# Performance work log

Measured on AMD Instinct MI355X. Metric: run time of the kernel, lower is better.

The kernel has to match this reference:

```python
import jax, jax.numpy as jnp
import numpy as np

NEIGHBOR_K = 3

def setup_inputs() -> dict:
    key = jax.random.key(0)
    k1, k2 = jax.random.split(key)
    query_fea = jax.random.normal(k1, (8, 75, 121, 640), dtype=jnp.float32)
    support_fea = jax.random.normal(k2, (8, 5, 5, 121, 640), dtype=jnp.float32)
    return {"query_fea": query_fea, "support_fea": support_fea}

def reference(query_fea, support_fea):
    # query_fea: [b, n_wq, patch_num, dim]
    # support_fea: [b, way, shot, patch_num, dim]
    b, way, shot, pn, dim = support_fea.shape
    sup = support_fea.reshape(b, way, shot * pn, dim)  # [b, way, S, dim]
    # inner products between every query patch and every support patch
    # sim: [b, n_wq, way, patch_num, S]
    sim = jnp.einsum('bqpd,bwsd->bqwps', query_fea, sup)
    # top-k over support patches (last axis), then mean over all topk values
    topk = jax.lax.top_k(sim, NEIGHBOR_K)[0]  # [b, n_wq, way, patch_num, k]
    return jnp.mean(topk, axis=(-2, -1))  # [b, n_wq, way]
```

## Files before the change

kernel.cpp:

```cpp
#include <hip/hip_runtime.h>
#include <hip/hip_bf16.h>

#define BATCH 8
#define NQ    75
#define WAY   5
#define PN    121
#define DIM   640
#define SSZ   605
#define TOPK  3

#define TM 128
#define TN 128
#define BK 64
#define NCH 5
#define KCH 10
#define QSTR 72

#define WSQ_ELEMS ((size_t)BATCH * NQ * TM * DIM)
#define WSS_ELEMS ((size_t)BATCH * WAY * 640 * DIM)
#define WS_NEED   ((WSQ_ELEMS + WSS_ELEMS) * 2)

typedef __attribute__((ext_vector_type(8))) short   short8;
typedef __attribute__((ext_vector_type(8))) __bf16  bf16x8;
typedef __attribute__((ext_vector_type(4))) float   f32x4;

__device__ inline unsigned short f2bf(float f) {
  unsigned u = __builtin_bit_cast(unsigned, f);
  return (unsigned short)((u + 0x7fffu + ((u >> 16) & 1u)) >> 16);
}

__device__ inline void ins3(float &a, float &b, float &c, float v) {
  float na = fmaxf(a, v);
  float nb = __builtin_amdgcn_fmed3f(v, a, b);
  float nc2 = __builtin_amdgcn_fmed3f(v, b, c);
  a = na; b = nb; c = nc2;
}


__global__ __launch_bounds__(256) void cvt_q(const float* __restrict__ qf,
                                             unsigned short* __restrict__ dst) {
  int idx = blockIdx.x * 256 + threadIdx.x;
  int c4  = idx % 160;
  int row = (idx / 160) & 127;
  int bq  = idx / (160 * 128);
  float4 v = make_float4(0.f, 0.f, 0.f, 0.f);
  if (row < PN)
    v = *reinterpret_cast<const float4*>(qf + ((size_t)(bq * PN + row) * DIM + c4 * 4));
  ushort4 h;
  h.x = f2bf(v.x); h.y = f2bf(v.y); h.z = f2bf(v.z); h.w = f2bf(v.w);
  *reinterpret_cast<ushort4*>(dst + (size_t)idx * 4) = h;
}

__global__ __launch_bounds__(256) void cvt_s(const float* __restrict__ sf,
                                             unsigned short* __restrict__ dst) {
  int idx = blockIdx.x * 256 + threadIdx.x;
  int c4  = idx % 160;
  int row = (idx / 160) % 640;
  int bw  = idx / (160 * 640);
  float4 v = make_float4(0.f, 0.f, 0.f, 0.f);
  if (row < SSZ)
    v = *reinterpret_cast<const float4*>(sf + ((size_t)(bw * SSZ + row) * DIM + c4 * 4));
  ushort4 h;
  h.x = f2bf(v.x); h.y = f2bf(v.y); h.z = f2bf(v.z); h.w = f2bf(v.w);
  *reinterpret_cast<ushort4*>(dst + (size_t)idx * 4) = h;
}


__global__ __launch_bounds__(256) void lpc_main(
    const short* __restrict__ wq,
    const short* __restrict__ wsp,
    float* __restrict__ out)
{
  __shared__ short Qs[TM][QSTR];
  __shared__ short Ss[TN][QSTR];
  __shared__ float t3row[TM][TOPK];
  __shared__ float red[4];

  const int bid = blockIdx.x;
  const int w   = bid % WAY;
  const int bq  = bid / WAY;
  const int b   = bid / (WAY * NQ);

  const short* Qb = wq  + (size_t)bq * TM * DIM;
  const short* Sb = wsp + (size_t)(b * WAY + w) * 640 * DIM;

  const int tid  = threadIdx.x;
  const int lane = tid & 63;
  const int wv   = tid >> 6;
  const int l15  = lane & 15;
  const int quad = lane >> 4;

  float t0[2][4], t1[2][4], t2[2][4];
  #pragma unroll
  for (int mt = 0; mt < 2; ++mt)
    #pragma unroll
    for (int r = 0; r < 4; ++r) {
      t0[mt][r] = -3.0e38f; t1[mt][r] = -3.0e38f; t2[mt][r] = -3.0e38f;
    }

  for (int nc = 0; nc < NCH; ++nc) {
    f32x4 acc[2][8];
    #pragma unroll
    for (int mt = 0; mt < 2; ++mt)
      #pragma unroll
      for (int nt = 0; nt < 8; ++nt)
        acc[mt][nt] = (f32x4){0.f, 0.f, 0.f, 0.f};

    for (int kc = 0; kc < KCH; ++kc) {
      const int kbase = kc * BK;
      __syncthreads();

      #pragma unroll
      for (int i = 0; i < 4; ++i) {
        int lin = i * 256 + tid;
        int row = lin >> 3;
        int ch  = lin & 7;
        float4 v = *reinterpret_cast<const float4*>(Qb + (size_t)row * DIM + kbase + ch * 8);
        *reinterpret_cast<float4*>(&Qs[row][ch * 8]) = v;
      }
      #pragma unroll
      for (int i = 0; i < 4; ++i) {
        int lin = i * 256 + tid;
        int row = lin >> 3;
        int ch  = lin & 7;
        float4 v = *reinterpret_cast<const float4*>(Sb + (size_t)(nc * TN + row) * DIM + kbase + ch * 8);
        *reinterpret_cast<float4*>(&Ss[row][ch * 8]) = v;
      }
      __syncthreads();

      #pragma unroll
      for (int kk = 0; kk < 2; ++kk) {
        bf16x8 a0 = __builtin_bit_cast(bf16x8,
            *reinterpret_cast<const short8*>(&Qs[wv * 32 +  0 + l15][kk * 32 + quad * 8]));
        bf16x8 a1 = __builtin_bit_cast(bf16x8,
            *reinterpret_cast<const short8*>(&Qs[wv * 32 + 16 + l15][kk * 32 + quad * 8]));
        #pragma unroll
        for (int nt = 0; nt < 8; ++nt) {
          bf16x8 bb = __builtin_bit_cast(bf16x8,
              *reinterpret_cast<const short8*>(&Ss[nt * 16 + l15][kk * 32 + quad * 8]));
          acc[0][nt] = __builtin_amdgcn_mfma_f32_16x16x32_bf16(a0, bb, acc[0][nt], 0, 0, 0);
          acc[1][nt] = __builtin_amdgcn_mfma_f32_16x16x32_bf16(a1, bb, acc[1][nt], 0, 0, 0);
        }
      }
    }

    #pragma unroll
    for (int nt = 0; nt < 8; ++nt) {
      int col = nc * TN + nt * 16 + l15;
      bool valid = col < SSZ;
      #pragma unroll
      for (int mt = 0; mt < 2; ++mt)
        #pragma unroll
        for (int r = 0; r < 4; ++r) {
          float v = valid ? acc[mt][nt][r] : -3.0e38f;
          ins3(t0[mt][r], t1[mt][r], t2[mt][r], v);
        }
    }
  }

  #pragma unroll
  for (int m = 1; m < 16; m <<= 1) {
    #pragma unroll
    for (int mt = 0; mt < 2; ++mt)
      #pragma unroll
      for (int r = 0; r < 4; ++r) {
        float o0 = __shfl_xor(t0[mt][r], m);
        float o1 = __shfl_xor(t1[mt][r], m);
        float o2 = __shfl_xor(t2[mt][r], m);
        ins3(t0[mt][r], t1[mt][r], t2[mt][r], o0);
        ins3(t0[mt][r], t1[mt][r], t2[mt][r], o1);
        ins3(t0[mt][r], t1[mt][r], t2[mt][r], o2);
      }
  }
  __syncthreads();
  if (l15 == 0) {
    #pragma unroll
    for (int mt = 0; mt < 2; ++mt)
      #pragma unroll
      for (int r = 0; r < 4; ++r) {
        int row = wv * 32 + mt * 16 + quad * 4 + r;
        t3row[row][0] = t0[mt][r];
        t3row[row][1] = t1[mt][r];
        t3row[row][2] = t2[mt][r];
      }
  }
  __syncthreads();

  float s = 0.f;
  for (int i = tid; i < PN * TOPK; i += 256)
    s += t3row[i / TOPK][i % TOPK];
  #pragma unroll
  for (int off = 32; off > 0; off >>= 1)
    s += __shfl_down(s, off);
  if (lane == 0) red[wv] = s;
  __syncthreads();
  if (tid == 0)
    out[bid] = (red[0] + red[1] + red[2] + red[3]) * (1.0f / (PN * TOPK));
}


#define FTN 64
#define FQSTR 72
#define FCSTR 67

__global__ __launch_bounds__(256) void lpc_fallback(
    const float* __restrict__ qf, const float* __restrict__ sf,
    float* __restrict__ out)
{
  __shared__ short Qs[TM][FQSTR];
  __shared__ short Ss[FTN][FQSTR];
  __shared__ float Cs[TM][FCSTR];
  __shared__ float top3[TM][TOPK];
  __shared__ float red[4];

  const int bid = blockIdx.x;
  const int w   = bid % WAY;
  const int qi  = (bid / WAY) % NQ;
  const int b   = bid / (WAY * NQ);
  const float* Qb = qf + ((size_t)(b * NQ + qi)) * PN * DIM;
  const float* Sb = sf + ((size_t)(b * WAY + w)) * SSZ * DIM;
  const int tid  = threadIdx.x;
  const int lane = tid & 63;
  const int wv   = tid >> 6;
  const int l15  = lane & 15;
  const int quad = lane >> 4;

  if (tid < TM) { top3[tid][0] = -3.0e38f; top3[tid][1] = -3.0e38f; top3[tid][2] = -3.0e38f; }
  f32x4 acc[2][4];
  for (int nc = 0; nc < 10; ++nc) {
    const int sbase = nc * FTN;
    int vn = SSZ - sbase; if (vn > FTN) vn = FTN;
    #pragma unroll
    for (int mt = 0; mt < 2; ++mt)
      #pragma unroll
      for (int nt = 0; nt < 4; ++nt) acc[mt][nt] = (f32x4){0.f,0.f,0.f,0.f};
    for (int kc = 0; kc < KCH; ++kc) {
      const int kbase = kc * BK;
      __syncthreads();
      #pragma unroll
      for (int i = 0; i < 8; ++i) {
        int lin = i * 256 + tid; int row = lin >> 4; int c4 = lin & 15;
        float4 v = make_float4(0.f,0.f,0.f,0.f);
        if (row < PN) v = *reinterpret_cast<const float4*>(Qb + (size_t)row * DIM + kbase + c4 * 4);
        ushort4 h; h.x=f2bf(v.x); h.y=f2bf(v.y); h.z=f2bf(v.z); h.w=f2bf(v.w);
        *reinterpret_cast<ushort4*>(&Qs[row][c4*4]) = h;
      }
      #pragma unroll
      for (int i = 0; i < 4; ++i) {
        int lin = i * 256 + tid; int row = lin >> 4; int c4 = lin & 15;
        int srow = sbase + row;
        float4 v = make_float4(0.f,0.f,0.f,0.f);
        if (srow < SSZ) v = *reinterpret_cast<const float4*>(Sb + (size_t)srow * DIM + kbase + c4 * 4);
        ushort4 h; h.x=f2bf(v.x); h.y=f2bf(v.y); h.z=f2bf(v.z); h.w=f2bf(v.w);
        *reinterpret_cast<ushort4*>(&Ss[row][c4*4]) = h;
      }
      __syncthreads();
      #pragma unroll
      for (int kk = 0; kk < 2; ++kk) {
        bf16x8 a0 = __builtin_bit_cast(bf16x8, *reinterpret_cast<const short8*>(&Qs[wv*32+ 0+l15][kk*32+quad*8]));
        bf16x8 a1 = __builtin_bit_cast(bf16x8, *reinterpret_cast<const short8*>(&Qs[wv*32+16+l15][kk*32+quad*8]));
        #pragma unroll
        for (int nt = 0; nt < 4; ++nt) {
          bf16x8 bb = __builtin_bit_cast(bf16x8, *reinterpret_cast<const short8*>(&Ss[nt*16+l15][kk*32+quad*8]));
          acc[0][nt] = __builtin_amdgcn_mfma_f32_16x16x32_bf16(a0, bb, acc[0][nt], 0,0,0);
          acc[1][nt] = __builtin_amdgcn_mfma_f32_16x16x32_bf16(a1, bb, acc[1][nt], 0,0,0);
        }
      }
    }
    #pragma unroll
    for (int mt = 0; mt < 2; ++mt)
      #pragma unroll
      for (int nt = 0; nt < 4; ++nt)
        #pragma unroll
        for (int r = 0; r < 4; ++r)
          Cs[wv*32+mt*16+quad*4+r][nt*16+l15] = acc[mt][nt][r];
    __syncthreads();
    {
      int row = tid >> 1; int half = tid & 1;
      float a = -3.0e38f, bb2 = -3.0e38f, c = -3.0e38f;
      int c0 = half * 32; int cend = c0 + 32; if (cend > vn) cend = vn;
      for (int cc = c0; cc < cend; ++cc) ins3(a, bb2, c, Cs[row][cc]);
      float o0 = __shfl_xor(a,1), o1 = __shfl_xor(bb2,1), o2 = __shfl_xor(c,1);
      ins3(a,bb2,c,o0); ins3(a,bb2,c,o1); ins3(a,bb2,c,o2);
      if (half == 0) {
        float r0=top3[row][0], r1=top3[row][1], r2=top3[row][2];
        ins3(r0,r1,r2,a); ins3(r0,r1,r2,bb2); ins3(r0,r1,r2,c);
        top3[row][0]=r0; top3[row][1]=r1; top3[row][2]=r2;
      }
    }
    __syncthreads();
  }
  float s = 0.f;
  for (int i = tid; i < PN * TOPK; i += 256) s += top3[i/TOPK][i%TOPK];
  #pragma unroll
  for (int off = 32; off > 0; off >>= 1) s += __shfl_down(s, off);
  if (lane == 0) red[wv] = s;
  __syncthreads();
  if (tid == 0) out[bid] = (red[0]+red[1]+red[2]+red[3]) * (1.0f/(PN*TOPK));
}


extern "C" void kernel_launch(void* const* d_in, const int* in_sizes, int n_in,
                              void* d_out, int out_size, void* d_ws, size_t ws_size,
                              hipStream_t stream) {
  const float* qf = (const float*)d_in[0];
  const float* sf = (const float*)d_in[1];
  float* out = (float*)d_out;
  (void)in_sizes; (void)n_in; (void)out_size;

  if (ws_size >= WS_NEED && d_ws != nullptr) {
    unsigned short* wq = (unsigned short*)d_ws;
    unsigned short* ws = wq + WSQ_ELEMS;
    cvt_q<<<48000, 256, 0, stream>>>(qf, wq);
    cvt_s<<<16000, 256, 0, stream>>>(sf, ws);
    lpc_main<<<BATCH * NQ * WAY, 256, 0, stream>>>((const short*)wq, (const short*)ws, out);
  } else {
    lpc_fallback<<<BATCH * NQ * WAY, 256, 0, stream>>>(qf, sf, out);
  }
}
```

Baseline: 773.4 us.

## Pre-swizzle bf16 tiles and stream them to LDS via direct global-to-LDS loads

```diff
diff --git a/kernel.cpp b/kernel.cpp
--- a/kernel.cpp
+++ b/kernel.cpp
@@ -9,16 +9,14 @@
 #define SSZ   605
 #define TOPK  3
 
-#define TM 128
-#define TN 128
-#define BK 64
+#define KCH 10
 #define NCH 5
-#define KCH 10
-#define QSTR 72
-
-#define WSQ_ELEMS ((size_t)BATCH * NQ * TM * DIM)
-#define WSS_ELEMS ((size_t)BATCH * WAY * 640 * DIM)
-#define WS_NEED   ((WSQ_ELEMS + WSS_ELEMS) * 2)
+
+#define NQCH  (600 * 10 * 128 * 8)
+#define NSCH  (40 * 5 * 10 * 128 * 8)
+#define TOTCH (NQCH + NSCH)
+#define WSQ_BYTES ((size_t)NQCH * 16)
+#define WS_NEED   ((size_t)TOTCH * 16)
 
 typedef __attribute__((ext_vector_type(8))) short   short8;
 typedef __attribute__((ext_vector_type(8))) __bf16  bf16x8;
@@ -30,50 +28,69 @@
 }
 
 __device__ inline void ins3(float &a, float &b, float &c, float v) {
-  float na = fmaxf(a, v);
-  float nb = __builtin_amdgcn_fmed3f(v, a, b);
+  float na  = fmaxf(a, v);
+  float nb  = __builtin_amdgcn_fmed3f(v, a, b);
   float nc2 = __builtin_amdgcn_fmed3f(v, b, c);
   a = na; b = nb; c = nc2;
 }
 
-
-__global__ __launch_bounds__(256) void cvt_q(const float* __restrict__ qf,
-                                             unsigned short* __restrict__ dst) {
+__device__ inline void async_copy16(const void* g, void* l) {
+  __builtin_amdgcn_global_load_lds(
+      (const __attribute__((address_space(1))) unsigned int*)g,
+      (__attribute__((address_space(3))) unsigned int*)l, 16, 0, 0);
+}
+
+__global__ __launch_bounds__(256) void cvt_pack(const float* __restrict__ qf,
+                                                const float* __restrict__ sf,
+                                                unsigned short* __restrict__ wq,
+                                                unsigned short* __restrict__ wsp) {
   int idx = blockIdx.x * 256 + threadIdx.x;
-  int c4  = idx % 160;
-  int row = (idx / 160) & 127;
-  int bq  = idx / (160 * 128);
-  float4 v = make_float4(0.f, 0.f, 0.f, 0.f);
-  if (row < PN)
-    v = *reinterpret_cast<const float4*>(qf + ((size_t)(bq * PN + row) * DIM + c4 * 4));
-  ushort4 h;
-  h.x = f2bf(v.x); h.y = f2bf(v.y); h.z = f2bf(v.z); h.w = f2bf(v.w);
-  *reinterpret_cast<ushort4*>(dst + (size_t)idx * 4) = h;
-}
-
-__global__ __launch_bounds__(256) void cvt_s(const float* __restrict__ sf,
-                                             unsigned short* __restrict__ dst) {
-  int idx = blockIdx.x * 256 + threadIdx.x;
-  int c4  = idx % 160;
-  int row = (idx / 160) % 640;
-  int bw  = idx / (160 * 640);
-  float4 v = make_float4(0.f, 0.f, 0.f, 0.f);
-  if (row < SSZ)
-    v = *reinterpret_cast<const float4*>(sf + ((size_t)(bw * SSZ + row) * DIM + c4 * 4));
-  ushort4 h;
-  h.x = f2bf(v.x); h.y = f2bf(v.y); h.z = f2bf(v.z); h.w = f2bf(v.w);
-  *reinterpret_cast<ushort4*>(dst + (size_t)idx * 4) = h;
-}
-
+  union { ushort4 h[2]; uint4 v; } o;
+  o.v = make_uint4(0u, 0u, 0u, 0u);
+  if (idx < NQCH) {
+    int p   = idx & 7;
+    int row = (idx >> 3) & 127;
+    int t   = idx >> 10;
+    int kc  = t % KCH;
+    int bq  = t / KCH;
+    int c   = p ^ (row & 7);
+    if (row < PN) {
+      const float* g = qf + ((size_t)bq * PN + row) * DIM + kc * 64 + c * 8;
+      float4 v0 = reinterpret_cast<const float4*>(g)[0];
+      float4 v1 = reinterpret_cast<const float4*>(g)[1];
+      o.h[0] = make_ushort4(f2bf(v0.x), f2bf(v0.y), f2bf(v0.z), f2bf(v0.w));
+      o.h[1] = make_ushort4(f2bf(v1.x), f2bf(v1.y), f2bf(v1.z), f2bf(v1.w));
+    }
+    reinterpret_cast<uint4*>(wq)[idx] = o.v;
+  } else if (idx < TOTCH) {
+    int si  = idx - NQCH;
+    int p   = si & 7;
+    int row = (si >> 3) & 127;
+    int t   = si >> 10;
+    int kc  = t % KCH;
+    int u   = t / KCH;
+    int nc  = u % NCH;
+    int bw  = u / NCH;
+    int srow = nc * 128 + row;
+    int c   = p ^ (row & 7);
+    if (srow < SSZ) {
+      const float* g = sf + ((size_t)bw * SSZ + srow) * DIM + kc * 64 + c * 8;
+      float4 v0 = reinterpret_cast<const float4*>(g)[0];
+      float4 v1 = reinterpret_cast<const float4*>(g)[1];
+      o.h[0] = make_ushort4(f2bf(v0.x), f2bf(v0.y), f2bf(v0.z), f2bf(v0.w));
+      o.h[1] = make_ushort4(f2bf(v1.x), f2bf(v1.y), f2bf(v1.z), f2bf(v1.w));
+    }
+    reinterpret_cast<uint4*>(wsp)[si] = o.v;
+  }
+}
 
 __global__ __launch_bounds__(256) void lpc_main(
-    const short* __restrict__ wq,
-    const short* __restrict__ wsp,
+    const char* __restrict__ wq,
+    const char* __restrict__ wsp,
     float* __restrict__ out)
 {
-  __shared__ short Qs[TM][QSTR];
-  __shared__ short Ss[TN][QSTR];
-  __shared__ float t3row[TM][TOPK];
+  __shared__ char Qs[16384];
+  __shared__ char Ss[16384];
   __shared__ float red[4];
 
   const int bid = blockIdx.x;
@@ -81,79 +98,85 @@
   const int bq  = bid / WAY;
   const int b   = bid / (WAY * NQ);
 
-  const short* Qb = wq  + (size_t)bq * TM * DIM;
-  const short* Sb = wsp + (size_t)(b * WAY + w) * 640 * DIM;
+  const char* Qtiles = wq  + (size_t)bq * KCH * 16384;
+  const char* Stiles = wsp + (size_t)(b * WAY + w) * NCH * KCH * 16384;
 
   const int tid  = threadIdx.x;
   const int lane = tid & 63;
   const int wv   = tid >> 6;
   const int l15  = lane & 15;
   const int quad = lane >> 4;
-
-  float t0[2][4], t1[2][4], t2[2][4];
+  const int mrow0 = (wv >> 1) * 64;
+  const int ncol0 = (wv & 1) * 64;
+
+  const int sw16 = (l15 & 7) * 16;
+  const int cp0  = (quad * 16) ^ sw16;
+  const int cp1  = ((4 + quad) * 16) ^ sw16;
+
+  const char* qb = Qs + (mrow0 + l15) * 128;
+  const char* sb = Ss + (ncol0 + l15) * 128;
+
+  float t3a[4][4], t3b[4][4], t3c[4][4];
   #pragma unroll
-  for (int mt = 0; mt < 2; ++mt)
+  for (int mt = 0; mt < 4; ++mt)
     #pragma unroll
     for (int r = 0; r < 4; ++r) {
-      t0[mt][r] = -3.0e38f; t1[mt][r] = -3.0e38f; t2[mt][r] = -3.0e38f;
+      t3a[mt][r] = -3.0e38f; t3b[mt][r] = -3.0e38f; t3c[mt][r] = -3.0e38f;
     }
 
   for (int nc = 0; nc < NCH; ++nc) {
-    f32x4 acc[2][8];
-    #pragma unroll
-    for (int mt = 0; mt < 2; ++mt)
-      #pragma unroll
-      for (int nt = 0; nt < 8; ++nt)
+    f32x4 acc[4][4];
+    #pragma unroll
+    for (int mt = 0; mt < 4; ++mt)
+      #pragma unroll
+      for (int nt = 0; nt < 4; ++nt)
         acc[mt][nt] = (f32x4){0.f, 0.f, 0.f, 0.f};
 
+    #pragma unroll 1
     for (int kc = 0; kc < KCH; ++kc) {
-      const int kbase = kc * BK;
       __syncthreads();
-
-      #pragma unroll
-      for (int i = 0; i < 4; ++i) {
-        int lin = i * 256 + tid;
-        int row = lin >> 3;
-        int ch  = lin & 7;
-        float4 v = *reinterpret_cast<const float4*>(Qb + (size_t)row * DIM + kbase + ch * 8);
-        *reinterpret_cast<float4*>(&Qs[row][ch * 8]) = v;
-      }
-      #pragma unroll
-      for (int i = 0; i < 4; ++i) {
-        int lin = i * 256 + tid;
-        int row = lin >> 3;
-        int ch  = lin & 7;
-        float4 v = *reinterpret_cast<const float4*>(Sb + (size_t)(nc * TN + row) * DIM + kbase + ch * 8);
-        *reinterpret_cast<float4*>(&Ss[row][ch * 8]) = v;
+      {
+        const char* qsl = Qtiles + (size_t)kc * 16384;
+        const char* ssl = Stiles + ((size_t)nc * KCH + kc) * 16384;
+        #pragma unroll
+        for (int i = 0; i < 4; ++i) {
+          int ch = wv * 4 + i;
+          async_copy16(qsl + ch * 1024 + lane * 16, Qs + ch * 1024);
+          async_copy16(ssl + ch * 1024 + lane * 16, Ss + ch * 1024);
+        }
       }
       __syncthreads();
 
       #pragma unroll
       for (int kk = 0; kk < 2; ++kk) {
-        bf16x8 a0 = __builtin_bit_cast(bf16x8,
-            *reinterpret_cast<const short8*>(&Qs[wv * 32 +  0 + l15][kk * 32 + quad * 8]));
-        bf16x8 a1 = __builtin_bit_cast(bf16x8,
-            *reinterpret_cast<const short8*>(&Qs[wv * 32 + 16 + l15][kk * 32 + quad * 8]));
-        #pragma unroll
-        for (int nt = 0; nt < 8; ++nt) {
-          bf16x8 bb = __builtin_bit_cast(bf16x8,
-              *reinterpret_cast<const short8*>(&Ss[nt * 16 + l15][kk * 32 + quad * 8]));
-          acc[0][nt] = __builtin_amdgcn_mfma_f32_16x16x32_bf16(a0, bb, acc[0][nt], 0, 0, 0);
-          acc[1][nt] = __builtin_amdgcn_mfma_f32_16x16x32_bf16(a1, bb, acc[1][nt], 0, 0, 0);
-        }
-      }
-    }
-
-    #pragma unroll
-    for (int nt = 0; nt < 8; ++nt) {
-      int col = nc * TN + nt * 16 + l15;
+        const int cp = kk ? cp1 : cp0;
+        short8 a[4], bf[4];
+        #pragma unroll
+        for (int mt = 0; mt < 4; ++mt)
+          a[mt] = *reinterpret_cast<const short8*>(qb + mt * 2048 + cp);
+        #pragma unroll
+        for (int nt = 0; nt < 4; ++nt)
+          bf[nt] = *reinterpret_cast<const short8*>(sb + nt * 2048 + cp);
+        #pragma unroll
+        for (int mt = 0; mt < 4; ++mt)
+          #pragma unroll
+          for (int nt = 0; nt < 4; ++nt)
+            acc[mt][nt] = __builtin_amdgcn_mfma_f32_16x16x32_bf16(
+                __builtin_bit_cast(bf16x8, a[mt]),
+                __builtin_bit_cast(bf16x8, bf[nt]), acc[mt][nt], 0, 0, 0);
+      }
+    }
+
+    #pragma unroll
+    for (int nt = 0; nt < 4; ++nt) {
+      int col = nc * 128 + ncol0 + nt * 16 + l15;
       bool valid = col < SSZ;
       #pragma unroll
-      for (int mt = 0; mt < 2; ++mt)
+      for (int mt = 0; mt < 4; ++mt)
         #pragma unroll
         for (int r = 0; r < 4; ++r) {
           float v = valid ? acc[mt][nt][r] : -3.0e38f;
-          ins3(t0[mt][r], t1[mt][r], t2[mt][r], v);
+          ins3(t3a[mt][r], t3b[mt][r], t3c[mt][r], v);
         }
     }
   }
@@ -161,56 +184,75 @@
   #pragma unroll
   for (int m = 1; m < 16; m <<= 1) {
     #pragma unroll
-    for (int mt = 0; mt < 2; ++mt)
+    for (int mt = 0; mt < 4; ++mt)
       #pragma unroll
       for (int r = 0; r < 4; ++r) {
-        float o0 = __shfl_xor(t0[mt][r], m);
-        float o1 = __shfl_xor(t1[mt][r], m);
-        float o2 = __shfl_xor(t2[mt][r], m);
-        ins3(t0[mt][r], t1[mt][r], t2[mt][r], o0);
-        ins3(t0[mt][r], t1[mt][r], t2[mt][r], o1);
-        ins3(t0[mt][r], t1[mt][r], t2[mt][r], o2);
-      }
-  }
-  __syncthreads();
-  if (l15 == 0) {
-    #pragma unroll
-    for (int mt = 0; mt < 2; ++mt)
+        float o0 = __shfl_xor(t3a[mt][r], m);
+        float o1 = __shfl_xor(t3b[mt][r], m);
+        float o2 = __shfl_xor(t3c[mt][r], m);
+        ins3(t3a[mt][r], t3b[mt][r], t3c[mt][r], o0);
+        ins3(t3a[mt][r], t3b[mt][r], t3c[mt][r], o1);
+        ins3(t3a[mt][r], t3b[mt][r], t3c[mt][r], o2);
+      }
+  }
+
+  float* tb = reinterpret_cast<float*>(Qs);
+  __syncthreads();
+  if ((wv & 1) == 1 && l15 == 0) {
+    #pragma unroll
+    for (int mt = 0; mt < 4; ++mt)
       #pragma unroll
       for (int r = 0; r < 4; ++r) {
-        int row = wv * 32 + mt * 16 + quad * 4 + r;
-        t3row[row][0] = t0[mt][r];
-        t3row[row][1] = t1[mt][r];
-        t3row[row][2] = t2[mt][r];
+        int row = mrow0 + mt * 16 + quad * 4 + r;
+        tb[row * 3 + 0] = t3a[mt][r];
+        tb[row * 3 + 1] = t3b[mt][r];
+        tb[row * 3 + 2] = t3c[mt][r];
+      }
+  }
+  __syncthreads();
+  if ((wv & 1) == 0 && l15 == 0) {
+    #pragma unroll
+    for (int mt = 0; mt < 4; ++mt)
+      #pragma unroll
+      for (int r = 0; r < 4; ++r) {
+        int row = mrow0 + mt * 16 + quad * 4 + r;
+        ins3(t3a[mt][r], t3b[mt][r], t3c[mt][r], tb[row * 3 + 0]);
+        ins3(t3a[mt][r], t3b[mt][r], t3c[mt][r], tb[row * 3 + 1]);
+        ins3(t3a[mt][r], t3b[mt][r], t3c[mt][r], tb[row * 3 + 2]);
+      }
+  }
+  __syncthreads();
+  if ((wv & 1) == 0 && l15 == 0) {
+    #pragma unroll
+    for (int mt = 0; mt < 4; ++mt)
+      #pragma unroll
+      for (int r = 0; r < 4; ++r) {
+        int row = mrow0 + mt * 16 + quad * 4 + r;
+        tb[row * 3 + 0] = t3a[mt][r];
+        tb[row * 3 + 1] = t3b[mt][r];
+        tb[row * 3 + 2] = t3c[mt][r];
       }
   }
   __syncthreads();
 
   float s = 0.f;
-  for (int i = tid; i < PN * TOPK; i += 256)
-    s += t3row[i / TOPK][i % TOPK];
+  for (int i = tid; i < PN * TOPK; i += 256) s += tb[i];
   #pragma unroll
-  for (int off = 32; off > 0; off >>= 1)
-    s += __shfl_down(s, off);
+  for (int off = 32; off > 0; off >>= 1) s += __shfl_down(s, off);
   if (lane == 0) red[wv] = s;
   __syncthreads();
   if (tid == 0)
     out[bid] = (red[0] + red[1] + red[2] + red[3]) * (1.0f / (PN * TOPK));
 }
-
-
-#define FTN 64
-#define FQSTR 72
-#define FCSTR 67
 
 __global__ __launch_bounds__(256) void lpc_fallback(
     const float* __restrict__ qf, const float* __restrict__ sf,
     float* __restrict__ out)
 {
-  __shared__ short Qs[TM][FQSTR];
-  __shared__ short Ss[FTN][FQSTR];
-  __shared__ float Cs[TM][FCSTR];
-  __shared__ float top3[TM][TOPK];
+  __shared__ short Qst[128][72];
+  __shared__ short Sst[64][72];
+  __shared__ float Cs[128][67];
+  __shared__ float top3[128][TOPK];
   __shared__ float red[4];
 
   const int bid = blockIdx.x;
@@ -225,17 +267,17 @@
   const int l15  = lane & 15;
   const int quad = lane >> 4;
 
-  if (tid < TM) { top3[tid][0] = -3.0e38f; top3[tid][1] = -3.0e38f; top3[tid][2] = -3.0e38f; }
+  if (tid < 128) { top3[tid][0] = -3.0e38f; top3[tid][1] = -3.0e38f; top3[tid][2] = -3.0e38f; }
   f32x4 acc[2][4];
   for (int nc = 0; nc < 10; ++nc) {
-    const int sbase = nc * FTN;
-    int vn = SSZ - sbase; if (vn > FTN) vn = FTN;
+    const int sbase = nc * 64;
+    int vn = SSZ - sbase; if (vn > 64) vn = 64;
     #pragma unroll
     for (int mt = 0; mt < 2; ++mt)
       #pragma unroll
       for (int nt = 0; nt < 4; ++nt) acc[mt][nt] = (f32x4){0.f,0.f,0.f,0.f};
     for (int kc = 0; kc < KCH; ++kc) {
-      const int kbase = kc * BK;
+      const int kbase = kc * 64;
       __syncthreads();
       #pragma unroll
       for (int i = 0; i < 8; ++i) {
@@ -243,7 +285,7 @@
         float4 v = make_float4(0.f,0.f,0.f,0.f);
         if (row < PN) v = *reinterpret_cast<const float4*>(Qb + (size_t)row * DIM + kbase + c4 * 4);
         ushort4 h; h.x=f2bf(v.x); h.y=f2bf(v.y); h.z=f2bf(v.z); h.w=f2bf(v.w);
-        *reinterpret_cast<ushort4*>(&Qs[row][c4*4]) = h;
+        *reinterpret_cast<ushort4*>(&Qst[row][c4*4]) = h;
       }
       #pragma unroll
       for (int i = 0; i < 4; ++i) {
@@ -252,16 +294,16 @@
         float4 v = make_float4(0.f,0.f,0.f,0.f);
         if (srow < SSZ) v = *reinterpret_cast<const float4*>(Sb + (size_t)srow * DIM + kbase + c4 * 4);
         ushort4 h; h.x=f2bf(v.x); h.y=f2bf(v.y); h.z=f2bf(v.z); h.w=f2bf(v.w);
-        *reinterpret_cast<ushort4*>(&Ss[row][c4*4]) = h;
+        *reinterpret_cast<ushort4*>(&Sst[row][c4*4]) = h;
       }
       __syncthreads();
       #pragma unroll
       for (int kk = 0; kk < 2; ++kk) {
-        bf16x8 a0 = __builtin_bit_cast(bf16x8, *reinterpret_cast<const short8*>(&Qs[wv*32+ 0+l15][kk*32+quad*8]));
-        bf16x8 a1 = __builtin_bit_cast(bf16x8, *reinterpret_cast<const short8*>(&Qs[wv*32+16+l15][kk*32+quad*8]));
+        bf16x8 a0 = __builtin_bit_cast(bf16x8, *reinterpret_cast<const short8*>(&Qst[wv*32+ 0+l15][kk*32+quad*8]));
+        bf16x8 a1 = __builtin_bit_cast(bf16x8, *reinterpret_cast<const short8*>(&Qst[wv*32+16+l15][kk*32+quad*8]));
         #pragma unroll
         for (int nt = 0; nt < 4; ++nt) {
-          bf16x8 bb = __builtin_bit_cast(bf16x8, *reinterpret_cast<const short8*>(&Ss[nt*16+l15][kk*32+quad*8]));
+          bf16x8 bb = __builtin_bit_cast(bf16x8, *reinterpret_cast<const short8*>(&Sst[nt*16+l15][kk*32+quad*8]));
           acc[0][nt] = __builtin_amdgcn_mfma_f32_16x16x32_bf16(a0, bb, acc[0][nt], 0,0,0);
           acc[1][nt] = __builtin_amdgcn_mfma_f32_16x16x32_bf16(a1, bb, acc[1][nt], 0,0,0);
         }
@@ -277,14 +319,14 @@
     __syncthreads();
     {
       int row = tid >> 1; int half = tid & 1;
-      float a = -3.0e38f, bb2 = -3.0e38f, c = -3.0e38f;
+      float a = -3.0e38f, b2 = -3.0e38f, c = -3.0e38f;
       int c0 = half * 32; int cend = c0 + 32; if (cend > vn) cend = vn;
-      for (int cc = c0; cc < cend; ++cc) ins3(a, bb2, c, Cs[row][cc]);
-      float o0 = __shfl_xor(a,1), o1 = __shfl_xor(bb2,1), o2 = __shfl_xor(c,1);
-      ins3(a,bb2,c,o0); ins3(a,bb2,c,o1); ins3(a,bb2,c,o2);
+      for (int cc = c0; cc < cend; ++cc) ins3(a, b2, c, Cs[row][cc]);
+      float o0 = __shfl_xor(a,1), o1 = __shfl_xor(b2,1), o2 = __shfl_xor(c,1);
+      ins3(a,b2,c,o0); ins3(a,b2,c,o1); ins3(a,b2,c,o2);
       if (half == 0) {
         float r0=top3[row][0], r1=top3[row][1], r2=top3[row][2];
-        ins3(r0,r1,r2,a); ins3(r0,r1,r2,bb2); ins3(r0,r1,r2,c);
+        ins3(r0,r1,r2,a); ins3(r0,r1,r2,b2); ins3(r0,r1,r2,c);
         top3[row][0]=r0; top3[row][1]=r1; top3[row][2]=r2;
       }
     }
@@ -298,7 +340,6 @@
   __syncthreads();
   if (tid == 0) out[bid] = (red[0]+red[1]+red[2]+red[3]) * (1.0f/(PN*TOPK));
 }
-
 
 extern "C" void kernel_launch(void* const* d_in, const int* in_sizes, int n_in,
                               void* d_out, int out_size, void* d_ws, size_t ws_size,
@@ -309,11 +350,10 @@
   (void)in_sizes; (void)n_in; (void)out_size;
 
   if (ws_size >= WS_NEED && d_ws != nullptr) {
-    unsigned short* wq = (unsigned short*)d_ws;
-    unsigned short* ws = wq + WSQ_ELEMS;
-    cvt_q<<<48000, 256, 0, stream>>>(qf, wq);
-    cvt_s<<<16000, 256, 0, stream>>>(sf, ws);
-    lpc_main<<<BATCH * NQ * WAY, 256, 0, stream>>>((const short*)wq, (const short*)ws, out);
+    unsigned short* wq  = (unsigned short*)d_ws;
+    unsigned short* wsp = wq + WSQ_BYTES / 2;
+    cvt_pack<<<TOTCH / 256, 256, 0, stream>>>(qf, sf, wq, wsp);
+    lpc_main<<<BATCH * NQ * WAY, 256, 0, stream>>>((const char*)wq, (const char*)wsp, out);
   } else {
     lpc_fallback<<<BATCH * NQ * WAY, 256, 0, stream>>>(qf, sf, out);
   }
```

Result: no change. 758.6 us (-1.9%).
